# Optimization experiments

Hardware: AMD Instinct MI355X
Metric: run time of the kernel (lower is better)

The kernel has to match this reference:

```python
import jax, jax.numpy as jnp
import numpy as np

TEMPERATURE = 0.5
EPS = 1e-8  # torch cosine_similarity norm clamp


def setup_inputs() -> dict:
    key = jax.random.key(0)
    k1, k2, k3 = jax.random.split(key, 3)
    N, D = 4096, 256
    z_i = jax.random.normal(k1, (N, D), dtype=jnp.float32)
    z_j = jax.random.normal(k2, (N, D), dtype=jnp.float32)
    weights = jax.random.uniform(k3, (N,), dtype=jnp.float32)
    return {"z_i": z_i, "z_j": z_j, "weights": weights}


def reference(z_i, z_j, weights):
    N = z_i.shape[0]
    z = jnp.concatenate([z_i, z_j], axis=0)  # [2N, D]
    # cosine similarity via normalized matmul (same math as broadcasted F.cosine_similarity)
    norm = jnp.maximum(jnp.linalg.norm(z, axis=1, keepdims=True), EPS)
    zn = z / norm
    sim = zn @ zn.T  # [2N, 2N]
    # positives: diagonals at offsets +N and -N
    sim_ij = jnp.diagonal(sim, offset=N)
    sim_ji = jnp.diagonal(sim, offset=-N)
    positives = jnp.concatenate([sim_ij, sim_ji], axis=0)  # [2N]
    mask = 1.0 - jnp.eye(2 * N, dtype=sim.dtype)
    denominator = jnp.sum(mask * jnp.exp(sim / TEMPERATURE), axis=1)  # [2N]
    numerator = jnp.exp(positives / TEMPERATURE)
    all_losses = -jnp.log(numerator / denominator)  # [2N]
    w2 = jnp.tile(weights, 2)  # weights.repeat(2)
    loss = jnp.sum(all_losses * w2) / jnp.sum(w2)
    return loss
```

## Files before the change

### kernel.cpp

```cpp
#include <hip/hip_runtime.h>
#include <hip/hip_bf16.h>

#define PN   4096
#define PN2  8192
#define PD   256
#define TILE 128
#define BK   64
#define NBLK (PN2 / TILE)
#define NTRI (NBLK * (NBLK + 1) / 2)

typedef __attribute__((ext_vector_type(8))) short bf16x8;
typedef __attribute__((ext_vector_type(4))) float f32x4;

typedef const __attribute__((address_space(1))) void* gas_ptr;
typedef __attribute__((address_space(3))) void* las_ptr;

__global__ __launch_bounds__(256) void normalize_kernel(
    const float* __restrict__ zi, const float* __restrict__ zj,
    __hip_bfloat16* __restrict__ zn, float* __restrict__ rowsum) {
  int r = blockIdx.x;
  int tid = threadIdx.x;
  const float* src = (r < PN) ? (zi + (size_t)r * PD) : (zj + (size_t)(r - PN) * PD);
  float x = src[tid];
  float s = x * x;
  #pragma unroll
  for (int off = 32; off >= 1; off >>= 1) s += __shfl_xor(s, off, 64);
  __shared__ float p[4];
  if ((tid & 63) == 0) p[tid >> 6] = s;
  __syncthreads();
  float tot = p[0] + p[1] + p[2] + p[3];
  float nrm = fmaxf(sqrtf(tot), 1e-8f);
  zn[(size_t)r * PD + tid] = __float2bfloat16(x / nrm);
  if (tid == 0) rowsum[r] = 0.0f;
}

__global__ __launch_bounds__(256) void simsum_kernel(
    const __hip_bfloat16* __restrict__ zn,
    float* __restrict__ rowsum, float* __restrict__ pos) {
  __shared__ char lds[2 * TILE * BK * 2];
  char* As = lds;
  char* Bs = lds + TILE * BK * 2;

  const int idx = blockIdx.x;
  int bj = (int)((sqrtf(8.0f * (float)idx + 1.0f) - 1.0f) * 0.5f);
  while ((bj + 1) * (bj + 2) / 2 <= idx) ++bj;
  while (bj * (bj + 1) / 2 > idx) --bj;
  const int bi = idx - bj * (bj + 1) / 2;
  const bool diagBlk = (bi == bj);
  const bool posBlk  = (bj == bi + PN / TILE);

  const int tid  = threadIdx.x;
  const int wave = tid >> 6;
  const int lane = tid & 63;
  const int quad = lane >> 4;
  const int c16  = lane & 15;
  const int rowBase = bi * TILE;
  const int colBase = bj * TILE;
  const int waveRow = (wave >> 1) * 64;
  const int waveCol = (wave & 1) * 64;

  f32x4 acc[4][4];
  #pragma unroll
  for (int i = 0; i < 4; ++i)
    #pragma unroll
    for (int j = 0; j < 4; ++j)
      acc[i][j] = (f32x4){0.f, 0.f, 0.f, 0.f};

  const int subrow = lane >> 3;
  const int slot   = lane & 7;
  const char* BsEff = diagBlk ? As : Bs;

  for (int kt = 0; kt < PD / BK; ++kt) {
    if (kt) __syncthreads();
    #pragma unroll
    for (int p = 0; p < 4; ++p) {
      int issue = wave * 4 + p;
      int r = issue * 8 + subrow;
      int c = slot ^ (r & 7);
      const __hip_bfloat16* ga = zn + (size_t)(rowBase + r) * PD + kt * BK + c * 8;
      __builtin_amdgcn_global_load_lds((gas_ptr)ga, (las_ptr)(As + issue * 1024), 16, 0, 0);
      if (!diagBlk) {
        const __hip_bfloat16* gb = zn + (size_t)(colBase + r) * PD + kt * BK + c * 8;
        __builtin_amdgcn_global_load_lds((gas_ptr)gb, (las_ptr)(Bs + issue * 1024), 16, 0, 0);
      }
    }
    __syncthreads();

    #pragma unroll
    for (int ki = 0; ki < 2; ++ki) {
      bf16x8 a[4], b[4];
      #pragma unroll
      for (int mi = 0; mi < 4; ++mi) {
        int r = waveRow + mi * 16 + c16;
        int ch = quad + ki * 4;
        a[mi] = *(const bf16x8*)(As + r * 128 + ((ch ^ (r & 7)) * 16));
      }
      #pragma unroll
      for (int ni = 0; ni < 4; ++ni) {
        int r = waveCol + ni * 16 + c16;
        int ch = quad + ki * 4;
        b[ni] = *(const bf16x8*)(BsEff + r * 128 + ((ch ^ (r & 7)) * 16));
      }
      #pragma unroll
      for (int mi = 0; mi < 4; ++mi)
        #pragma unroll
        for (int ni = 0; ni < 4; ++ni)
          acc[mi][ni] = __builtin_amdgcn_mfma_f32_16x16x32_bf16(a[mi], b[ni], acc[mi][ni], 0, 0, 0);
    }
  }

  float colsum[4] = {0.f, 0.f, 0.f, 0.f};
  #pragma unroll
  for (int mi = 0; mi < 4; ++mi) {
    int rbase = rowBase + waveRow + mi * 16 + quad * 4;
    float rs[4] = {0.f, 0.f, 0.f, 0.f};
    #pragma unroll
    for (int ni = 0; ni < 4; ++ni) {
      int gcol = colBase + waveCol + ni * 16 + c16;
      #pragma unroll
      for (int t = 0; t < 4; ++t) {
        int grow = rbase + t;
        float sim = acc[mi][ni][t];
        float e = __expf(2.0f * sim);
        if (diagBlk && gcol == grow) e = 0.0f;
        rs[t] += e;
        colsum[ni] += e;
        if (posBlk && gcol == grow + PN) {
          pos[grow] = sim;
          pos[grow + PN] = sim;
        }
      }
    }
    #pragma unroll
    for (int t = 0; t < 4; ++t) {
      #pragma unroll
      for (int off = 1; off <= 8; off <<= 1) rs[t] += __shfl_xor(rs[t], off, 64);
    }
    if (c16 == 0) {
      #pragma unroll
      for (int t = 0; t < 4; ++t) atomicAdd(&rowsum[rbase + t], rs[t]);
    }
  }
  if (!diagBlk) {
    #pragma unroll
    for (int ni = 0; ni < 4; ++ni) {
      float cs = colsum[ni];
      cs += __shfl_xor(cs, 16, 64);
      cs += __shfl_xor(cs, 32, 64);
      if (quad == 0) atomicAdd(&rowsum[colBase + waveCol + ni * 16 + c16], cs);
    }
  }
}

__global__ __launch_bounds__(1024) void finalize_kernel(
    const float* __restrict__ rowsum, const float* __restrict__ pos,
    const float* __restrict__ w, float* __restrict__ out) {
  int tid = threadIdx.x;
  float wl = 0.f, ws = 0.f;
  for (int i = tid; i < PN2; i += 1024) {
    float li = logf(rowsum[i]) - 2.0f * pos[i];
    float wi = w[i & (PN - 1)];
    wl += wi * li;
    ws += wi;
  }
  #pragma unroll
  for (int off = 32; off >= 1; off >>= 1) {
    wl += __shfl_xor(wl, off, 64);
    ws += __shfl_xor(ws, off, 64);
  }
  __shared__ float pl[16], pw[16];
  if ((tid & 63) == 0) { pl[tid >> 6] = wl; pw[tid >> 6] = ws; }
  __syncthreads();
  if (tid == 0) {
    float sl = 0.f, sw = 0.f;
    #pragma unroll
    for (int k = 0; k < 16; ++k) { sl += pl[k]; sw += pw[k]; }
    out[0] = sl / sw;
  }
}

extern "C" void kernel_launch(void* const* d_in, const int* in_sizes, int n_in,
                              void* d_out, int out_size, void* d_ws, size_t ws_size,
                              hipStream_t stream) {
  const float* zi = (const float*)d_in[0];
  const float* zj = (const float*)d_in[1];
  const float* w  = (const float*)d_in[2];
  float* out = (float*)d_out;

  __hip_bfloat16* zn = (__hip_bfloat16*)d_ws;
  float* rowsum = (float*)((char*)d_ws + (size_t)PN2 * PD * 2);
  float* pos = rowsum + PN2;

  normalize_kernel<<<PN2, 256, 0, stream>>>(zi, zj, zn, rowsum);
  simsum_kernel<<<NTRI, 256, 0, stream>>>(zn, rowsum, pos);
  finalize_kernel<<<1, 1024, 0, stream>>>(rowsum, pos, w, out);
}
```

Baseline: 108.6 us.

## Load MFMA operands directly from global memory, dropping LDS staging

The similarity GEMM kernel no longer stages A/B tiles through shared memory with global_load_lds and barriers. Each wave now loads its bf16x8 fragments straight from global memory (16-byte per-lane loads) for the full K=256 loop, fully unrolled. This removes LDS traffic and syncthreads. In exchange, rows shared between waves are fetched redundantly through the cache hierarchy, row-strided loads coalesce less well, and register pressure rises from the fully unrolled loop.

```diff
diff --git a/kernel.cpp b/kernel.cpp
--- a/kernel.cpp
+++ b/kernel.cpp
@@ -5,15 +5,11 @@
 #define PN2  8192
 #define PD   256
 #define TILE 128
-#define BK   64
 #define NBLK (PN2 / TILE)
 #define NTRI (NBLK * (NBLK + 1) / 2)
 
 typedef __attribute__((ext_vector_type(8))) short bf16x8;
 typedef __attribute__((ext_vector_type(4))) float f32x4;
-
-typedef const __attribute__((address_space(1))) void* gas_ptr;
-typedef __attribute__((address_space(3))) void* las_ptr;
 
 __global__ __launch_bounds__(256) void normalize_kernel(
     const float* __restrict__ zi, const float* __restrict__ zj,
@@ -37,10 +33,6 @@
 __global__ __launch_bounds__(256) void simsum_kernel(
     const __hip_bfloat16* __restrict__ zn,
     float* __restrict__ rowsum, float* __restrict__ pos) {
-  __shared__ char lds[2 * TILE * BK * 2];
-  char* As = lds;
-  char* Bs = lds + TILE * BK * 2;
-
   const int idx = blockIdx.x;
   int bj = (int)((sqrtf(8.0f * (float)idx + 1.0f) - 1.0f) * 0.5f);
   while ((bj + 1) * (bj + 2) / 2 <= idx) ++bj;
@@ -54,10 +46,16 @@
   const int lane = tid & 63;
   const int quad = lane >> 4;
   const int c16  = lane & 15;
-  const int rowBase = bi * TILE;
-  const int colBase = bj * TILE;
-  const int waveRow = (wave >> 1) * 64;
-  const int waveCol = (wave & 1) * 64;
+  const int wrow = bi * TILE + (wave >> 1) * 64;
+  const int wcol = bj * TILE + (wave & 1) * 64;
+
+  const __hip_bfloat16* aP[4];
+  const __hip_bfloat16* bP[4];
+  #pragma unroll
+  for (int i = 0; i < 4; ++i) {
+    aP[i] = zn + (size_t)(wrow + i * 16 + c16) * PD + quad * 8;
+    bP[i] = zn + (size_t)(wcol + i * 16 + c16) * PD + quad * 8;
+  }
 
   f32x4 acc[4][4];
   #pragma unroll
@@ -66,57 +64,28 @@
     for (int j = 0; j < 4; ++j)
       acc[i][j] = (f32x4){0.f, 0.f, 0.f, 0.f};
 
-  const int subrow = lane >> 3;
-  const int slot   = lane & 7;
-  const char* BsEff = diagBlk ? As : Bs;
-
-  for (int kt = 0; kt < PD / BK; ++kt) {
-    if (kt) __syncthreads();
+  #pragma unroll
+  for (int k = 0; k < PD; k += 32) {
+    bf16x8 a[4], b[4];
     #pragma unroll
-    for (int p = 0; p < 4; ++p) {
-      int issue = wave * 4 + p;
-      int r = issue * 8 + subrow;
-      int c = slot ^ (r & 7);
-      const __hip_bfloat16* ga = zn + (size_t)(rowBase + r) * PD + kt * BK + c * 8;
-      __builtin_amdgcn_global_load_lds((gas_ptr)ga, (las_ptr)(As + issue * 1024), 16, 0, 0);
-      if (!diagBlk) {
-        const __hip_bfloat16* gb = zn + (size_t)(colBase + r) * PD + kt * BK + c * 8;
-        __builtin_amdgcn_global_load_lds((gas_ptr)gb, (las_ptr)(Bs + issue * 1024), 16, 0, 0);
-      }
-    }
-    __syncthreads();
-
+    for (int mi = 0; mi < 4; ++mi) a[mi] = *(const bf16x8*)(aP[mi] + k);
     #pragma unroll
-    for (int ki = 0; ki < 2; ++ki) {
-      bf16x8 a[4], b[4];
+    for (int ni = 0; ni < 4; ++ni) b[ni] = *(const bf16x8*)(bP[ni] + k);
+    #pragma unroll
+    for (int mi = 0; mi < 4; ++mi)
       #pragma unroll
-      for (int mi = 0; mi < 4; ++mi) {
-        int r = waveRow + mi * 16 + c16;
-        int ch = quad + ki * 4;
-        a[mi] = *(const bf16x8*)(As + r * 128 + ((ch ^ (r & 7)) * 16));
-      }
-      #pragma unroll
-      for (int ni = 0; ni < 4; ++ni) {
-        int r = waveCol + ni * 16 + c16;
-        int ch = quad + ki * 4;
-        b[ni] = *(const bf16x8*)(BsEff + r * 128 + ((ch ^ (r & 7)) * 16));
-      }
-      #pragma unroll
-      for (int mi = 0; mi < 4; ++mi)
-        #pragma unroll
-        for (int ni = 0; ni < 4; ++ni)
-          acc[mi][ni] = __builtin_amdgcn_mfma_f32_16x16x32_bf16(a[mi], b[ni], acc[mi][ni], 0, 0, 0);
-    }
+      for (int ni = 0; ni < 4; ++ni)
+        acc[mi][ni] = __builtin_amdgcn_mfma_f32_16x16x32_bf16(a[mi], b[ni], acc[mi][ni], 0, 0, 0);
   }
 
   float colsum[4] = {0.f, 0.f, 0.f, 0.f};
   #pragma unroll
   for (int mi = 0; mi < 4; ++mi) {
-    int rbase = rowBase + waveRow + mi * 16 + quad * 4;
+    int rbase = wrow + mi * 16 + quad * 4;
     float rs[4] = {0.f, 0.f, 0.f, 0.f};
     #pragma unroll
     for (int ni = 0; ni < 4; ++ni) {
-      int gcol = colBase + waveCol + ni * 16 + c16;
+      int gcol = wcol + ni * 16 + c16;
       #pragma unroll
       for (int t = 0; t < 4; ++t) {
         int grow = rbase + t;
@@ -147,7 +116,7 @@
       float cs = colsum[ni];
       cs += __shfl_xor(cs, 16, 64);
       cs += __shfl_xor(cs, 32, 64);
-      if (quad == 0) atomicAdd(&rowsum[colBase + waveCol + ni * 16 + c16], cs);
+      if (quad == 0) atomicAdd(&rowsum[wcol + ni * 16 + c16], cs);
     }
   }
 }
```

Result: slower. 143.8 us (+32.3%).
